# Kernel tuning notes

Hardware: AMD Instinct MI355X
Metric: run time of the kernel (lower is better)

## Reference

```python
import jax, jax.numpy as jnp
import numpy as np

N = 10000        # nodes
E = 320000       # edges (avg degree 32)
W = 256          # width (assert width >= 256)
H = 8            # num_head (RESCALE_EDGE assumed (1,1) -> nhead=8, dhead=32)
D = W // H       # per-head dim
BOND = 33        # EMBED_BOND[0]
BAG = 3          # indices per edge bag
EPS_GN = 1e-5


def setup_inputs() -> dict:
    key = jax.random.key(0)
    ks = jax.random.split(key, 12)
    x = jax.random.normal(ks[0], (N, W), dtype=jnp.float32)
    edge_idx = jax.random.randint(ks[1], (2, E), 0, N)
    edge_attr = jax.random.randint(ks[2], (E, BAG), 0, BOND)
    # node in-degree wrt scatter target edge_idx[1], clamped to >= 1
    deg = jax.ops.segment_sum(jnp.ones((E,), jnp.float32), edge_idx[1], num_segments=N)
    deg = jnp.maximum(deg, 1.0)
    s = 1.0 / np.sqrt(W)
    W_src = jax.random.normal(ks[3], (W, W), dtype=jnp.float32) * s
    W_tgt = jax.random.normal(ks[4], (W, W), dtype=jnp.float32) * s
    emb = jax.random.normal(ks[5], (BOND, W), dtype=jnp.float32) * 0.02
    emb = emb.at[0].set(0.0)  # padding_idx=0 row is zeros
    sd = 1.0 / np.sqrt(D)
    W_gate = jax.random.normal(ks[6], (H, D, D), dtype=jnp.float32) * sd  # grouped conv1d k=1
    W_val = jax.random.normal(ks[7], (H, D, D), dtype=jnp.float32) * sd
    W_post = jax.random.normal(ks[8], (W, W), dtype=jnp.float32) * s
    deg_param = jnp.zeros((W,), jnp.float32) - 0.01  # DegreeLayer degree_init
    return {"x": x, "deg": deg, "edge_idx": edge_idx, "edge_attr": edge_attr,
            "W_src": W_src, "W_tgt": W_tgt, "emb": emb,
            "W_gate": W_gate, "W_val": W_val, "W_post": W_post,
            "deg_param": deg_param}


def reference(x, deg, edge_idx, edge_attr, W_src, W_tgt, emb, W_gate, W_val, W_post, deg_param):
    # src/tgt 1x1 Conv1d == per-node linear, then edge gather
    xs = x @ W_src.T                      # [N, W]
    xt = x @ W_tgt.T                      # [N, W]
    xx = xs[edge_idx[0]] + xt[edge_idx[1]]  # [E, W]

    # EmbeddingBag(mode='mean', padding_idx=0): padded entries excluded
    mask = (edge_attr != 0).astype(xx.dtype)            # [E, BAG]
    bag = jnp.einsum('ebc,eb->ec', emb[edge_attr], mask)  # [E, W]
    cnt = jnp.maximum(mask.sum(-1, keepdims=True), 1.0)
    gate_bias = bag / cnt

    # GroupNorm(H, W, affine=False) over [E, W, 1]
    xg = xx.reshape(-1, H, D)
    mu = xg.mean(-1, keepdims=True)
    var = xg.var(-1, keepdims=True)
    xn = (xg - mu) / jnp.sqrt(var + EPS_GN)              # [E, H, D]

    # gated grouped 1x1 convs (dropout is identity at eval)
    gin = xn + gate_bias.reshape(-1, H, D)
    gate = jax.nn.relu(jnp.einsum('ehd,hfd->ehf', gin, W_gate))
    val = jnp.einsum('ehd,hfd->ehf', xn, W_val)
    act = (gate * val).reshape(-1, W)                    # [E, W]
    out_e = act @ W_post.T                               # [E, W]

    # scatter-sum to nodes, then degree rescale
    agg = jax.ops.segment_sum(out_e, edge_idx[1], num_segments=x.shape[0])
    return jnp.power(deg[:, None], deg_param) * agg      # [N, W]
```

## Files before the change

kernel.cpp:

```cpp
#include <hip/hip_runtime.h>

#define WID 256
#define EPS_GN 1e-5f

typedef __bf16 v8bf __attribute__((ext_vector_type(8)));
typedef __bf16 v2bf __attribute__((ext_vector_type(2)));
typedef float  v4f  __attribute__((ext_vector_type(4)));
typedef float  v2f  __attribute__((ext_vector_type(2)));

__device__ inline unsigned short f2b(float f) {
    unsigned int u = __builtin_bit_cast(unsigned int, f);
    unsigned int r = (u + 0x7fffu + ((u >> 16) & 1u)) >> 16;
    return (unsigned short)r;
}
__device__ inline float lo16(unsigned int u) { return __builtin_bit_cast(float, u << 16); }
__device__ inline float hi16(unsigned int u) { return __builtin_bit_cast(float, u & 0xffff0000u); }
__device__ inline v2f unpk(unsigned int u) {
    v2f r; r.x = lo16(u); r.y = hi16(u); return r;
}

__device__ inline v2f pk_add(v2f a, v2f b) {
    v2f d; asm("v_pk_add_f32 %0, %1, %2" : "=v"(d) : "v"(a), "v"(b)); return d;
}
__device__ inline v2f pk_mul(v2f a, v2f b) {
    v2f d; asm("v_pk_mul_f32 %0, %1, %2" : "=v"(d) : "v"(a), "v"(b)); return d;
}
__device__ inline v2f pk_fma(v2f a, v2f b, v2f c) {
    v2f d; asm("v_pk_fma_f32 %0, %1, %2, %3" : "=v"(d) : "v"(a), "v"(b), "v"(c)); return d;
}

#if __has_builtin(__builtin_amdgcn_cvt_pk_bf16_f32)
__device__ inline unsigned int pkbf(float a, float b) {
    v2bf r = __builtin_amdgcn_cvt_pk_bf16_f32(a, b);
    return __builtin_bit_cast(unsigned int, r);
}
#else
__device__ inline unsigned int pkbf(float a, float b) {
    return (unsigned int)f2b(a) | ((unsigned int)f2b(b) << 16);
}
#endif

#if __has_builtin(__builtin_amdgcn_fdot2_f32_bf16)
__device__ inline float pairsum(unsigned int u, float s) {
    v2bf p = __builtin_bit_cast(v2bf, u);
    v2bf ones = __builtin_bit_cast(v2bf, 0x3f803f80u);
    return __builtin_amdgcn_fdot2_f32_bf16(p, ones, s, false);
}
#else
__device__ inline float pairsum(unsigned int u, float s) {
    return s + lo16(u) + hi16(u);
}
#endif

__global__ void cast_k(const float* __restrict__ Wsrc, const float* __restrict__ Wtgt,
                       const float* __restrict__ Wp, const float* __restrict__ Wg,
                       const float* __restrict__ Wv, const float* __restrict__ emb,
                       const int* __restrict__ eidx,
                       unsigned short* __restrict__ Wsb, unsigned short* __restrict__ Wtb,
                       unsigned short* __restrict__ Wpb, unsigned short* __restrict__ Wgb,
                       unsigned short* __restrict__ Wvb, unsigned short* __restrict__ embWgT,
                       int* __restrict__ cnt, int* __restrict__ ssrc,
                       int* __restrict__ stgt, int* __restrict__ sattr,
                       int N, int BOND, int E, int NT32) {
    int i = blockIdx.x * 256 + threadIdx.x;
    int gsz = gridDim.x * 256;
    for (int j = E + i; j < NT32; j += gsz) { ssrc[j] = 0; stgt[j] = 0; sattr[j] = 0; }
    for (int j = i; j < E; j += gsz) atomicAdd(&cnt[eidx[E + j]], 1);
    {
        const float2* s2 = (const float2*)Wsrc;
        const float2* t2 = (const float2*)Wtgt;
        const float2* p2 = (const float2*)Wp;
        unsigned int* so = (unsigned int*)Wsb;
        unsigned int* to = (unsigned int*)Wtb;
        unsigned int* po = (unsigned int*)Wpb;
        for (int j = i; j < 32768; j += gsz) {
            float2 a = s2[j], b = t2[j], c = p2[j];
            so[j] = pkbf(a.x, a.y); to[j] = pkbf(b.x, b.y); po[j] = pkbf(c.x, c.y);
        }
    }
    {
        const float2* g2 = (const float2*)Wg;
        const float2* v2p = (const float2*)Wv;
        unsigned int* go = (unsigned int*)Wgb;
        unsigned int* vo = (unsigned int*)Wvb;
        for (int j = i; j < 4096; j += gsz) {
            float2 a = g2[j], b = v2p[j];
            go[j] = pkbf(a.x, a.y); vo[j] = pkbf(b.x, b.y);
        }
    }
    for (int j = i; j < 8192; j += gsz) {
        int jr = j >> 5, k = j & 31;
        int kk = k ? k : 32;
        float sacc = 0.f;
        if (kk < BOND) {
            int h = jr >> 5, f = jr & 31;
            const float4* er = (const float4*)(emb + (size_t)kk * WID + h * 32);
            const float4* wr = (const float4*)(Wg + h * 1024 + f * 32);
#pragma unroll
            for (int d = 0; d < 8; d++) {
                float4 e4 = er[d], w4 = wr[d];
                sacc += e4.x * w4.x + e4.y * w4.y + e4.z * w4.z + e4.w * w4.w;
            }
        }
        embWgT[jr * 32 + k] = f2b(sacc);
    }
}

__global__ void scan_k(const int* __restrict__ cnt, int* __restrict__ cur, int N) {
    __shared__ int buf[10240];
    __shared__ int wsum[16];
    int t = threadIdx.x;
    int C = (N + 1023) >> 10;
    int M = C << 10;
    for (int i = t; i < M; i += 1024) buf[i] = (i < N) ? cnt[i] : 0;
    __syncthreads();
    int base0 = t * C;
    int s = 0;
    for (int i = 0; i < C; i++) s += buf[base0 + i];
    int lane = t & 63, wv = t >> 6;
    int v = s;
#pragma unroll
    for (int d = 1; d < 64; d <<= 1) {
        int u = __shfl_up(v, d);
        if (lane >= d) v += u;
    }
    if (lane == 63) wsum[wv] = v;
    __syncthreads();
    if (wv == 0 && lane < 16) {
        int x = wsum[lane];
#pragma unroll
        for (int d = 1; d < 16; d <<= 1) {
            int u = __shfl_up(x, d, 16);
            if (lane >= d) x += u;
        }
        wsum[lane] = x;
    }
    __syncthreads();
    int waveoff = (wv == 0) ? 0 : wsum[wv - 1];
    int base = waveoff + (v - s);
    for (int i = 0; i < C; i++) {
        int val = buf[base0 + i];
        buf[base0 + i] = base;
        base += val;
    }
    __syncthreads();
    for (int i = t; i < N; i += 1024) cur[i] = buf[i];
}

__global__ __launch_bounds__(256, 2)
void prepproj_k(const float* __restrict__ x, const unsigned short* __restrict__ Wsb,
                const unsigned short* __restrict__ Wtb, const int* __restrict__ eidx,
                const int* __restrict__ eattr, int* __restrict__ cur,
                int* __restrict__ ssrc, int* __restrict__ stgt, int* __restrict__ sattr,
                unsigned short* __restrict__ xsb, unsigned short* __restrict__ xtb,
                int N, int E, int PB, int AUX) {
    __shared__ unsigned short ab[32 * 264];
    int t = threadIdx.x, b = blockIdx.x;

    if (b >= PB) {
        int atid = (b - PB) * 256 + t, asz = AUX * 256;
        for (int i = atid; i < E; i += asz) {
            int tg = eidx[E + i];
            int p = atomicAdd(&cur[tg], 1);
            ssrc[p] = eidx[i];
            stgt[p] = tg;
            const int* ap = eattr + (size_t)i * 3;
            sattr[p] = (ap[0] & 63) | ((ap[1] & 63) << 6) | ((ap[2] & 63) << 12);
        }
        return;
    }

    int n0 = b * 32;
#pragma unroll
    for (int ch = 0; ch < 8; ch++) {
        int flat = ch * 1024 + t * 4;
        int row = flat >> 8, col = flat & 255;
        int n = n0 + row;
        float4 v = (n < N) ? *(const float4*)&x[(size_t)n * WID + col]
                           : make_float4(0.f, 0.f, 0.f, 0.f);
        *(uint2*)&ab[row * 264 + col] = make_uint2(pkbf(v.x, v.y), pkbf(v.z, v.w));
    }
    __syncthreads();
    int w = t >> 6, lane = t & 63, m = lane & 15, kg = lane >> 4;
#pragma unroll
    for (int pass = 0; pass < 2; pass++) {
        const unsigned short* Wb = pass ? Wtb : Wsb;
        unsigned short* outp = pass ? xtb : xsb;
        v4f acc[2][4];
#pragma unroll
        for (int mt = 0; mt < 2; mt++)
#pragma unroll
            for (int nt = 0; nt < 4; nt++) acc[mt][nt] = (v4f){0.f, 0.f, 0.f, 0.f};
#pragma unroll
        for (int kt = 0; kt < 8; kt++) {
            int k0 = kt * 32 + kg * 8;
            v8bf a0 = *(const v8bf*)&ab[m * 264 + k0];
            v8bf a1 = *(const v8bf*)&ab[(16 + m) * 264 + k0];
#pragma unroll
            for (int nt = 0; nt < 4; nt++) {
                int j = w * 64 + nt * 16 + m;
                v8bf bfr = *(const v8bf*)&Wb[j * 256 + k0];
                acc[0][nt] = __builtin_amdgcn_mfma_f32_16x16x32_bf16(bfr, a0, acc[0][nt], 0, 0, 0);
                acc[1][nt] = __builtin_amdgcn_mfma_f32_16x16x32_bf16(bfr, a1, acc[1][nt], 0, 0, 0);
            }
        }
#pragma unroll
        for (int mt = 0; mt < 2; mt++) {
            int n = n0 + mt * 16 + m;
            if (n < N) {
#pragma unroll
                for (int nt = 0; nt < 4; nt++) {
                    int j0 = w * 64 + nt * 16 + kg * 4;
                    *(uint2*)&outp[(size_t)n * WID + j0] =
                        make_uint2(pkbf(acc[mt][nt][0], acc[mt][nt][1]),
                                   pkbf(acc[mt][nt][2], acc[mt][nt][3]));
                }
            }
        }
    }
}

__global__ __launch_bounds__(256, 8)
void edge_k(const unsigned short* __restrict__ xsb, const unsigned short* __restrict__ xtb,
            const int* __restrict__ ssrc, const int* __restrict__ stgt,
            const int* __restrict__ sattr, const unsigned short* __restrict__ Wgb,
            const unsigned short* __restrict__ Wvb, const unsigned short* __restrict__ embWgT,
            float* __restrict__ aggact, int E, int NT, int PER) {
    __shared__ unsigned short xxb[8704];
    __shared__ unsigned short Mld[32 * 40];
    __shared__ int src_s[32], tgt_s[32];
    __shared__ int segmask_s;

    int tile = (blockIdx.x & 7) * PER + (blockIdx.x >> 3);
    if (tile >= NT) return;
    int t = threadIdx.x;
    int e0 = tile * 32;
    int ne = min(32, E - e0);

    {
        int tgtv = -1;
        if (t < 32) {
            int e = e0 + t;
            src_s[t] = ssrc[e];
            int tg = stgt[e];
            tgt_s[t] = tg;
            int pa = sattr[e];
            uint4* Mr = (uint4*)&Mld[t * 40];
#pragma unroll
            for (int q = 0; q < 4; q++) Mr[q] = make_uint4(0u, 0u, 0u, 0u);
            int a0 = pa & 63, a1 = (pa >> 6) & 63, a2 = (pa >> 12) & 63;
            int c = (a0 != 0) + (a1 != 0) + (a2 != 0);
            float inv = (c > 0) ? 1.f / (float)c : 0.f;
            float wa = inv * (float)(1 + (a1 == a0) + (a2 == a0));
            float wb = inv * (float)(1 + (a2 == a1));
            if (a0) Mld[t * 40 + (a0 & 31)] = f2b(wa);
            if (a1 && a1 != a0) Mld[t * 40 + (a1 & 31)] = f2b(wb);
            if (a2 && a2 != a0 && a2 != a1) Mld[t * 40 + (a2 & 31)] = f2b(inv);
            tgtv = (t < ne) ? tg : -1;
        }
        if (t < 64) {
            int nxt = __shfl_down(tgtv, 1);
            bool flag = (t < ne) && ((t == ne - 1) || (nxt != tgtv));
            unsigned long long bal = __ballot(flag);
            if (t == 0) segmask_s = (int)(unsigned int)bal;
        }
    }
    __syncthreads();

    {
        int e = t >> 3, c = t & 7;
        int sn = src_s[e], g = tgt_s[e];
        const uint4* ps = (const uint4*)(xsb + (size_t)sn * WID);
        const uint4* pt = (const uint4*)(xtb + (size_t)g * WID);
        uint4 us[4], ut[4];
#pragma unroll
        for (int i = 0; i < 4; i++) { us[i] = ps[c + 8 * i]; ut[i] = pt[c + 8 * i]; }
        v2f v2[4][4];
        float sum[4], sq[4];
#pragma unroll
        for (int i = 0; i < 4; i++) {
            const unsigned int* au = (const unsigned int*)&us[i];
            const unsigned int* bu = (const unsigned int*)&ut[i];
            v2f s2 = (v2f){0.f, 0.f}, q2 = (v2f){0.f, 0.f};
#pragma unroll
            for (int q = 0; q < 4; q++) {
                v2f a = pk_add(unpk(au[q]), unpk(bu[q]));
                v2[i][q] = a;
                s2 = pk_add(s2, a);
                q2 = pk_fma(a, a, q2);
            }
            sum[i] = s2.x + s2.y;
            sq[i]  = q2.x + q2.y;
        }
#pragma unroll
        for (int mask = 1; mask <= 2; mask <<= 1)
#pragma unroll
            for (int i = 0; i < 4; i++) {
                sum[i] += __shfl_xor(sum[i], mask);
                sq[i]  += __shfl_xor(sq[i], mask);
            }
#pragma unroll
        for (int i = 0; i < 4; i++) {
            float mu = sum[i] * (1.f / 32.f);
            float var = sq[i] * (1.f / 32.f) - mu * mu;
            float rs = rsqrtf(var + EPS_GN);
            float nmr = -mu * rs;
            v2f rs2 = (v2f){rs, rs}, nm2 = (v2f){nmr, nmr};
            unsigned int pk[4];
#pragma unroll
            for (int q = 0; q < 4; q++) {
                v2f r = pk_fma(v2[i][q], rs2, nm2);
                pk[q] = pkbf(r.x, r.y);
            }
            *(uint4*)&xxb[e * 264 + (c + 8 * i) * 8] = make_uint4(pk[0], pk[1], pk[2], pk[3]);
        }
    }
    __syncthreads();

    {
        int w = t >> 6, lane = t & 63, m = lane & 15, kg = lane >> 4;
        v8bf axn[2][2], aM[2];
#pragma unroll
        for (int mt = 0; mt < 2; mt++) {
            int row = mt * 16 + m;
            axn[0][mt] = *(const v8bf*)&xxb[row * 264 + (w * 2 + 0) * 32 + kg * 8];
            axn[1][mt] = *(const v8bf*)&xxb[row * 264 + (w * 2 + 1) * 32 + kg * 8];
            aM[mt] = *(const v8bf*)&Mld[row * 40 + kg * 8];
        }
        __syncthreads();
        v4f z = {0.f, 0.f, 0.f, 0.f};
#pragma unroll
        for (int hh = 0; hh < 2; hh++) {
            int h = w * 2 + hh;
#pragma unroll
            for (int nt = 0; nt < 2; nt++) {
                int fj = nt * 16 + m;
                int j = h * 32 + fj;
                v8bf bWg = *(const v8bf*)&Wgb[h * 1024 + fj * 32 + kg * 8];
                v8bf bWv = *(const v8bf*)&Wvb[h * 1024 + fj * 32 + kg * 8];
                v8bf bE  = *(const v8bf*)&embWgT[j * 32 + kg * 8];
#pragma unroll
                for (int mt = 0; mt < 2; mt++) {
                    v4f cgm = __builtin_amdgcn_mfma_f32_16x16x32_bf16(axn[hh][mt], bWg, z, 0, 0, 0);
                    cgm = __builtin_amdgcn_mfma_f32_16x16x32_bf16(aM[mt], bE, cgm, 0, 0, 0);
                    v4f cv = __builtin_amdgcn_mfma_f32_16x16x32_bf16(axn[hh][mt], bWv, z, 0, 0, 0);
                    v2f g0 = (v2f){fmaxf(cgm[0], 0.f), fmaxf(cgm[1], 0.f)};
                    v2f g1 = (v2f){fmaxf(cgm[2], 0.f), fmaxf(cgm[3], 0.f)};
                    g0 = pk_mul(g0, (v2f){cv[0], cv[1]});
                    g1 = pk_mul(g1, (v2f){cv[2], cv[3]});
                    int e0i = mt * 16 + kg * 4;
                    *(unsigned int*)&xxb[j * 34 + e0i]     = pkbf(g0.x, g0.y);
                    *(unsigned int*)&xxb[j * 34 + e0i + 2] = pkbf(g1.x, g1.y);
                }
            }
        }
    }
    __syncthreads();

    {
        unsigned int mask = (unsigned int)__builtin_amdgcn_readfirstlane(segmask_s);
        float sum = 0.f;
#pragma unroll
        for (int i = 0; i < 16; i++) {
            unsigned int r = *(const unsigned int*)&xxb[t * 34 + 2 * i];
            if (!((mask >> (2 * i)) & 1)) {
                sum = pairsum(r, sum);
                if ((mask >> (2 * i + 1)) & 1) {
                    int tg = __builtin_amdgcn_readfirstlane(tgt_s[2 * i + 1]);
                    atomicAdd(&aggact[(size_t)tg * WID + t], sum);
                    sum = 0.f;
                }
            } else {
                sum += lo16(r);
                int tg = __builtin_amdgcn_readfirstlane(tgt_s[2 * i]);
                atomicAdd(&aggact[(size_t)tg * WID + t], sum);
                sum = hi16(r);
                if ((mask >> (2 * i + 1)) & 1) {
                    int tg2 = __builtin_amdgcn_readfirstlane(tgt_s[2 * i + 1]);
                    atomicAdd(&aggact[(size_t)tg2 * WID + t], sum);
                    sum = 0.f;
                }
            }
        }
    }
}

__global__ __launch_bounds__(256, 2)
void post_k(const float* __restrict__ aggact, const unsigned short* __restrict__ Wpb,
            const float* __restrict__ deg, const float* __restrict__ dp,
            float* __restrict__ out, int N) {
    __shared__ unsigned short ab[32 * 264];
    __shared__ float degl[32];
    int t = threadIdx.x;
    int n0 = blockIdx.x * 32;
#pragma unroll
    for (int ch = 0; ch < 8; ch++) {
        int flat = ch * 1024 + t * 4;
        int row = flat >> 8, col = flat & 255;
        int n = n0 + row;
        float4 v = (n < N) ? *(const float4*)&aggact[(size_t)n * WID + col]
                           : make_float4(0.f, 0.f, 0.f, 0.f);
        *(uint2*)&ab[row * 264 + col] = make_uint2(pkbf(v.x, v.y), pkbf(v.z, v.w));
    }
    if (t < 32) {
        int n = n0 + t;
        degl[t] = (n < N) ? log2f(deg[n]) : 0.f;
    }
    __syncthreads();
    int w = t >> 6, lane = t & 63, m = lane & 15, kg = lane >> 4;
    v4f acc[2][4];
#pragma unroll
    for (int mt = 0; mt < 2; mt++)
#pragma unroll
        for (int nt = 0; nt < 4; nt++) acc[mt][nt] = (v4f){0.f, 0.f, 0.f, 0.f};
#pragma unroll
    for (int kt = 0; kt < 8; kt++) {
        int k0 = kt * 32 + kg * 8;
        v8bf a0 = *(const v8bf*)&ab[m * 264 + k0];
        v8bf a1 = *(const v8bf*)&ab[(16 + m) * 264 + k0];
#pragma unroll
        for (int nt = 0; nt < 4; nt++) {
            int j = w * 64 + nt * 16 + m;
            v8bf b = *(const v8bf*)&Wpb[j * 256 + k0];
            acc[0][nt] = __builtin_amdgcn_mfma_f32_16x16x32_bf16(b, a0, acc[0][nt], 0, 0, 0);
            acc[1][nt] = __builtin_amdgcn_mfma_f32_16x16x32_bf16(b, a1, acc[1][nt], 0, 0, 0);
        }
    }
#pragma unroll
    for (int mt = 0; mt < 2; mt++) {
        int n = n0 + mt * 16 + m;
        if (n < N) {
            float ld = degl[mt * 16 + m];
#pragma unroll
            for (int nt = 0; nt < 4; nt++) {
                int j0 = w * 64 + nt * 16 + kg * 4;
                float4 dv = *(const float4*)&dp[j0];
                float4 o;
                o.x = exp2f(dv.x * ld) * acc[mt][nt][0];
                o.y = exp2f(dv.y * ld) * acc[mt][nt][1];
                o.z = exp2f(dv.z * ld) * acc[mt][nt][2];
                o.w = exp2f(dv.w * ld) * acc[mt][nt][3];
                *(float4*)&out[(size_t)n * WID + j0] = o;
            }
        }
    }
}

extern "C" void kernel_launch(void* const* d_in, const int* in_sizes, int n_in,
                              void* d_out, int out_size, void* d_ws, size_t ws_size,
                              hipStream_t stream) {
    const float* x    = (const float*)d_in[0];
    const float* deg  = (const float*)d_in[1];
    const int*   eidx = (const int*)d_in[2];
    const int*   eatt = (const int*)d_in[3];
    const float* Wsrc = (const float*)d_in[4];
    const float* Wtgt = (const float*)d_in[5];
    const float* emb  = (const float*)d_in[6];
    const float* Wg   = (const float*)d_in[7];
    const float* Wv   = (const float*)d_in[8];
    const float* Wp   = (const float*)d_in[9];
    const float* dp   = (const float*)d_in[10];
    int N = in_sizes[0] / WID;
    int E = in_sizes[2] / 2;
    int BOND = in_sizes[6] / WID;

    int NT = (E + 31) / 32;
    int NT32 = NT * 32;

    float* ws     = (float*)d_ws;
    float* aggact = ws;
    int*   cnt    = (int*)(aggact + (size_t)N * WID);
    int*   cur    = cnt + N;
    int*   ssrc   = cur + N;
    int*   stgt   = ssrc + NT32;
    int*   sattr  = stgt + NT32;
    unsigned short* xsb = (unsigned short*)(sattr + NT32);
    unsigned short* xtb = xsb + (size_t)N * WID;
    unsigned short* Wsb = xtb + (size_t)N * WID;
    unsigned short* Wtb = Wsb + 65536;
    unsigned short* Wpb = Wtb + 65536;
    unsigned short* Wgb = Wpb + 65536;
    unsigned short* Wvb = Wgb + 8192;
    unsigned short* embWgT = Wvb + 8192;

    int PB = (N + 31) / 32;
    int AUX = 128;
    int PER = (NT + 7) / 8;

    hipMemsetAsync(aggact, 0, (size_t)N * WID * sizeof(float) + (size_t)N * sizeof(int),
                   stream);

    cast_k<<<640, 256, 0, stream>>>(Wsrc, Wtgt, Wp, Wg, Wv, emb, eidx,
                                    Wsb, Wtb, Wpb, Wgb, Wvb, embWgT,
                                    cnt, ssrc, stgt, sattr, N, BOND, E, NT32);
    scan_k<<<1, 1024, 0, stream>>>(cnt, cur, N);
    prepproj_k<<<PB + AUX, 256, 0, stream>>>(x, Wsb, Wtb, eidx, eatt, cur,
                                             ssrc, stgt, sattr, xsb, xtb,
                                             N, E, PB, AUX);
    edge_k<<<PER * 8, 256, 0, stream>>>(xsb, xtb, ssrc, stgt, sattr, Wgb, Wvb, embWgT,
                                        aggact, E, NT, PER);
    post_k<<<PB, 256, 0, stream>>>(aggact, Wpb, deg, dp, (float*)d_out, N);
}
```

Measured before the change: 214.0 us.

## Move weight casts into prepproj aux blocks and fuse src/tgt projection passes

Moves the W_post, gate/value weight casts and the emb·W_gate precompute out of cast_k into the auxiliary blocks of prepproj_k, so they run alongside the edge-sort scatter and off the serial cast_k/scan_k chain. cast_k is launched with half as many blocks. The projection kernel now computes the src and tgt products in one k-loop that shares each A-fragment load, which doubles accumulator registers per thread. The higher register use may reduce occupancy under the 2-blocks-per-SM launch bound.

```diff
diff --git a/kernel.cpp b/kernel.cpp
--- a/kernel.cpp
+++ b/kernel.cpp
@@ -53,15 +53,11 @@
 #endif
 
 __global__ void cast_k(const float* __restrict__ Wsrc, const float* __restrict__ Wtgt,
-                       const float* __restrict__ Wp, const float* __restrict__ Wg,
-                       const float* __restrict__ Wv, const float* __restrict__ emb,
                        const int* __restrict__ eidx,
                        unsigned short* __restrict__ Wsb, unsigned short* __restrict__ Wtb,
-                       unsigned short* __restrict__ Wpb, unsigned short* __restrict__ Wgb,
-                       unsigned short* __restrict__ Wvb, unsigned short* __restrict__ embWgT,
                        int* __restrict__ cnt, int* __restrict__ ssrc,
                        int* __restrict__ stgt, int* __restrict__ sattr,
-                       int N, int BOND, int E, int NT32) {
+                       int N, int E, int NT32) {
     int i = blockIdx.x * 256 + threadIdx.x;
     int gsz = gridDim.x * 256;
     for (int j = E + i; j < NT32; j += gsz) { ssrc[j] = 0; stgt[j] = 0; sattr[j] = 0; }
@@ -69,40 +65,12 @@
     {
         const float2* s2 = (const float2*)Wsrc;
         const float2* t2 = (const float2*)Wtgt;
-        const float2* p2 = (const float2*)Wp;
         unsigned int* so = (unsigned int*)Wsb;
         unsigned int* to = (unsigned int*)Wtb;
-        unsigned int* po = (unsigned int*)Wpb;
         for (int j = i; j < 32768; j += gsz) {
-            float2 a = s2[j], b = t2[j], c = p2[j];
-            so[j] = pkbf(a.x, a.y); to[j] = pkbf(b.x, b.y); po[j] = pkbf(c.x, c.y);
-        }
-    }
-    {
-        const float2* g2 = (const float2*)Wg;
-        const float2* v2p = (const float2*)Wv;
-        unsigned int* go = (unsigned int*)Wgb;
-        unsigned int* vo = (unsigned int*)Wvb;
-        for (int j = i; j < 4096; j += gsz) {
-            float2 a = g2[j], b = v2p[j];
-            go[j] = pkbf(a.x, a.y); vo[j] = pkbf(b.x, b.y);
-        }
-    }
-    for (int j = i; j < 8192; j += gsz) {
-        int jr = j >> 5, k = j & 31;
-        int kk = k ? k : 32;
-        float sacc = 0.f;
-        if (kk < BOND) {
-            int h = jr >> 5, f = jr & 31;
-            const float4* er = (const float4*)(emb + (size_t)kk * WID + h * 32);
-            const float4* wr = (const float4*)(Wg + h * 1024 + f * 32);
-#pragma unroll
-            for (int d = 0; d < 8; d++) {
-                float4 e4 = er[d], w4 = wr[d];
-                sacc += e4.x * w4.x + e4.y * w4.y + e4.z * w4.z + e4.w * w4.w;
-            }
-        }
-        embWgT[jr * 32 + k] = f2b(sacc);
+            float2 a = s2[j], b = t2[j];
+            so[j] = pkbf(a.x, a.y); to[j] = pkbf(b.x, b.y);
+        }
     }
 }
 
@@ -153,7 +121,11 @@
                 const int* __restrict__ eattr, int* __restrict__ cur,
                 int* __restrict__ ssrc, int* __restrict__ stgt, int* __restrict__ sattr,
                 unsigned short* __restrict__ xsb, unsigned short* __restrict__ xtb,
-                int N, int E, int PB, int AUX) {
+                const float* __restrict__ Wp, const float* __restrict__ Wg,
+                const float* __restrict__ Wv, const float* __restrict__ emb,
+                unsigned short* __restrict__ Wpb, unsigned short* __restrict__ Wgb,
+                unsigned short* __restrict__ Wvb, unsigned short* __restrict__ embWgT,
+                int N, int E, int PB, int AUX, int BOND) {
     __shared__ unsigned short ab[32 * 264];
     int t = threadIdx.x, b = blockIdx.x;
 
@@ -167,6 +139,40 @@
             const int* ap = eattr + (size_t)i * 3;
             sattr[p] = (ap[0] & 63) | ((ap[1] & 63) << 6) | ((ap[2] & 63) << 12);
         }
+        {
+            const float2* p2 = (const float2*)Wp;
+            unsigned int* po = (unsigned int*)Wpb;
+            for (int j = atid; j < 32768; j += asz) {
+                float2 c = p2[j];
+                po[j] = pkbf(c.x, c.y);
+            }
+        }
+        {
+            const float2* g2 = (const float2*)Wg;
+            const float2* v2p = (const float2*)Wv;
+            unsigned int* go = (unsigned int*)Wgb;
+            unsigned int* vo = (unsigned int*)Wvb;
+            for (int j = atid; j < 4096; j += asz) {
+                float2 a = g2[j], c = v2p[j];
+                go[j] = pkbf(a.x, a.y); vo[j] = pkbf(c.x, c.y);
+            }
+        }
+        for (int j = atid; j < 8192; j += asz) {
+            int jr = j >> 5, k = j & 31;
+            int kk = k ? k : 32;
+            float sacc = 0.f;
+            if (kk < BOND) {
+                int h = jr >> 5, f = jr & 31;
+                const float4* er = (const float4*)(emb + (size_t)kk * WID + h * 32);
+                const float4* wr = (const float4*)(Wg + h * 1024 + f * 32);
+#pragma unroll
+                for (int d = 0; d < 8; d++) {
+                    float4 e4 = er[d], w4 = wr[d];
+                    sacc += e4.x * w4.x + e4.y * w4.y + e4.z * w4.z + e4.w * w4.w;
+                }
+            }
+            embWgT[jr * 32 + k] = f2b(sacc);
+        }
         return;
     }
 
@@ -182,28 +188,32 @@
     }
     __syncthreads();
     int w = t >> 6, lane = t & 63, m = lane & 15, kg = lane >> 4;
-#pragma unroll
-    for (int pass = 0; pass < 2; pass++) {
-        const unsigned short* Wb = pass ? Wtb : Wsb;
-        unsigned short* outp = pass ? xtb : xsb;
-        v4f acc[2][4];
+    v4f acc[2][2][4];
+#pragma unroll
+    for (int p = 0; p < 2; p++)
 #pragma unroll
         for (int mt = 0; mt < 2; mt++)
 #pragma unroll
-            for (int nt = 0; nt < 4; nt++) acc[mt][nt] = (v4f){0.f, 0.f, 0.f, 0.f};
-#pragma unroll
-        for (int kt = 0; kt < 8; kt++) {
-            int k0 = kt * 32 + kg * 8;
-            v8bf a0 = *(const v8bf*)&ab[m * 264 + k0];
-            v8bf a1 = *(const v8bf*)&ab[(16 + m) * 264 + k0];
-#pragma unroll
-            for (int nt = 0; nt < 4; nt++) {
-                int j = w * 64 + nt * 16 + m;
-                v8bf bfr = *(const v8bf*)&Wb[j * 256 + k0];
-                acc[0][nt] = __builtin_amdgcn_mfma_f32_16x16x32_bf16(bfr, a0, acc[0][nt], 0, 0, 0);
-                acc[1][nt] = __builtin_amdgcn_mfma_f32_16x16x32_bf16(bfr, a1, acc[1][nt], 0, 0, 0);
-            }
-        }
+            for (int nt = 0; nt < 4; nt++) acc[p][mt][nt] = (v4f){0.f, 0.f, 0.f, 0.f};
+#pragma unroll
+    for (int kt = 0; kt < 8; kt++) {
+        int k0 = kt * 32 + kg * 8;
+        v8bf a0 = *(const v8bf*)&ab[m * 264 + k0];
+        v8bf a1 = *(const v8bf*)&ab[(16 + m) * 264 + k0];
+#pragma unroll
+        for (int nt = 0; nt < 4; nt++) {
+            int j = w * 64 + nt * 16 + m;
+            v8bf bs = *(const v8bf*)&Wsb[j * 256 + k0];
+            v8bf bt = *(const v8bf*)&Wtb[j * 256 + k0];
+            acc[0][0][nt] = __builtin_amdgcn_mfma_f32_16x16x32_bf16(bs, a0, acc[0][0][nt], 0, 0, 0);
+            acc[0][1][nt] = __builtin_amdgcn_mfma_f32_16x16x32_bf16(bs, a1, acc[0][1][nt], 0, 0, 0);
+            acc[1][0][nt] = __builtin_amdgcn_mfma_f32_16x16x32_bf16(bt, a0, acc[1][0][nt], 0, 0, 0);
+            acc[1][1][nt] = __builtin_amdgcn_mfma_f32_16x16x32_bf16(bt, a1, acc[1][1][nt], 0, 0, 0);
+        }
+    }
+#pragma unroll
+    for (int p = 0; p < 2; p++) {
+        unsigned short* outp = p ? xtb : xsb;
 #pragma unroll
         for (int mt = 0; mt < 2; mt++) {
             int n = n0 + mt * 16 + m;
@@ -212,8 +222,8 @@
                 for (int nt = 0; nt < 4; nt++) {
                     int j0 = w * 64 + nt * 16 + kg * 4;
                     *(uint2*)&outp[(size_t)n * WID + j0] =
-                        make_uint2(pkbf(acc[mt][nt][0], acc[mt][nt][1]),
-                                   pkbf(acc[mt][nt][2], acc[mt][nt][3]));
+                        make_uint2(pkbf(acc[p][mt][nt][0], acc[p][mt][nt][1]),
+                                   pkbf(acc[p][mt][nt][2], acc[p][mt][nt][3]));
                 }
             }
         }
@@ -490,13 +500,14 @@
     hipMemsetAsync(aggact, 0, (size_t)N * WID * sizeof(float) + (size_t)N * sizeof(int),
                    stream);
 
-    cast_k<<<640, 256, 0, stream>>>(Wsrc, Wtgt, Wp, Wg, Wv, emb, eidx,
-                                    Wsb, Wtb, Wpb, Wgb, Wvb, embWgT,
-                                    cnt, ssrc, stgt, sattr, N, BOND, E, NT32);
+    cast_k<<<320, 256, 0, stream>>>(Wsrc, Wtgt, eidx, Wsb, Wtb,
+                                    cnt, ssrc, stgt, sattr, N, E, NT32);
     scan_k<<<1, 1024, 0, stream>>>(cnt, cur, N);
     prepproj_k<<<PB + AUX, 256, 0, stream>>>(x, Wsb, Wtb, eidx, eatt, cur,
                                              ssrc, stgt, sattr, xsb, xtb,
-                                             N, E, PB, AUX);
+                                             Wp, Wg, Wv, emb,
+                                             Wpb, Wgb, Wvb, embWgT,
+                                             N, E, PB, AUX, BOND);
     edge_k<<<PER * 8, 256, 0, stream>>>(xsb, xtb, ssrc, stgt, sattr, Wgb, Wvb, embWgT,
                                         aggact, E, NT, PER);
     post_k<<<PB, 256, 0, stream>>>(aggact, Wpb, deg, dp, (float*)d_out, N);
```

Result: no change. 211.1 us (-1.3%).
